# Kernel optimization log

Hardware: AMD Instinct MI355X
Metric: run time of the kernel (lower is better)

Reference implementation:

```python
import jax, jax.numpy as jnp
import numpy as np

N, E, B, H, W = 2048, 65536, 4, 64, 64
D, ED, HID, ATT, STEPS = 128, 128, 256, 16, 4
NODE_IN, EDGE_IN = 256, 64


def setup_inputs() -> dict:
    key = jax.random.key(0)
    ks = jax.random.split(key, 24)
    p = lambda k, s: jax.random.normal(k, s, jnp.float32) * 0.05
    z = lambda n: jnp.zeros((n,), jnp.float32)
    return dict(
        x=jax.random.normal(ks[0], (N, NODE_IN), jnp.float32),
        edge_attr=jax.random.normal(ks[1], (E, EDGE_IN), jnp.float32),
        edge_index=jax.random.randint(ks[2], (2, E), 0, N),
        feature_maps=jax.random.normal(ks[3], (B, 32, H, W), jnp.float32),
        batch_index=jax.random.randint(ks[4], (N,), 0, B),
        ne_w=p(ks[5], (D, NODE_IN)), ne_b=z(D),
        ee_w=p(ks[6], (ED, EDGE_IN)), ee_b=z(ED),
        me_w1=p(ks[7], (HID, 2 * (D + ATT) + ED)), me_b1=z(HID),
        me_w2=p(ks[8], (ED, HID)), me_b2=z(ED),
        mn_w=p(ks[9], (D, D + ATT + ED)), mn_b=z(D),
        key_w=p(ks[10], (ATT, D)), key_b=z(ATT),
        q_w=p(ks[11], (ATT, 32)), q_b=z(ATT),
        v_w=p(ks[12], (ATT, 32)), v_b=z(ATT),
        ec_w1=p(ks[13], (64, ED)), ec_b1=z(64),
        ec_w2=p(ks[14], (1, 64)), ec_b2=z(1),
        nc_w1=p(ks[15], (64, D)), nc_b1=z(64),
        nc_w2=p(ks[16], (1, 64)), nc_b2=z(1),
        cl_w1=p(ks[17], (64, D)), cl_b1=z(64),
        cl_w2=p(ks[18], (17, 64)), cl_b2=z(17),
    )


def _forward(x, edge_attr, feature_maps, edge_index, batch_index,
             ne_w, ne_b, ee_w, ee_b, me_w1, me_b1, me_w2, me_b2, mn_w, mn_b,
             key_w, key_b, q_w, q_b, v_w, v_b,
             ec_w1, ec_b1, ec_w2, ec_b2, nc_w1, nc_b1, nc_w2, nc_b2,
             cl_w1, cl_b1, cl_w2, cl_b2):
    relu = jax.nn.relu
    node_features = relu(x @ ne_w.T + ne_b)            # [N, D]
    edge_features = relu(edge_attr @ ee_w.T + ee_b)    # [E, ED]
    fm = feature_maps.reshape(B, 32, H * W)
    queries = jnp.einsum('oc,bcp->bop', q_w, fm) + q_b[None, :, None]  # [B,ATT,HW]
    values = jnp.einsum('oc,bcp->bop', v_w, fm) + v_b[None, :, None]   # [B,ATT,HW]
    src, tgt = edge_index[0], edge_index[1]  # j, i (messages aggregated at i)
    node_ids = jnp.arange(N)
    for _ in range(STEPS):
        k = node_features @ key_w.T + key_b                        # [N, ATT]
        attn = jax.nn.softmax(jnp.einsum('nk,bkp->bnp', k, queries), axis=2)
        result = jnp.einsum('bkp,bnp->bkn', values, attn)          # [B, ATT, N]
        res = result[batch_index, :, node_ids]                     # [N, ATT]
        nf = jnp.concatenate([node_features, res], axis=1)         # [N, D+ATT]
        x_i, x_j = nf[tgt], nf[src]
        edge_features = relu(relu(jnp.concatenate([x_i, x_j, edge_features], 1) @ me_w1.T + me_b1) @ me_w2.T + me_b2)
        msg = relu(jnp.concatenate([x_i, edge_features], 1) @ mn_w.T + mn_b)
        node_features = jax.ops.segment_sum(msg, tgt, num_segments=N)
    pe = (relu(edge_features @ ec_w1.T + ec_b1) @ ec_w2.T + ec_b2).squeeze(-1)
    pn = (relu(node_features @ nc_w1.T + nc_b1) @ nc_w2.T + nc_b2).squeeze(-1)
    pc = relu(node_features @ cl_w1.T + cl_b1) @ cl_w2.T + cl_b2
    return pe, pn, pc, node_features, edge_features


def reference(x, edge_attr, edge_index, feature_maps, batch_index,
              ne_w, ne_b, ee_w, ee_b, me_w1, me_b1, me_w2, me_b2, mn_w, mn_b,
              key_w, key_b, q_w, q_b, v_w, v_b,
              ec_w1, ec_b1, ec_w2, ec_b2, nc_w1, nc_b1, nc_w2, nc_b2,
              cl_w1, cl_b1, cl_w2, cl_b2):
    return _forward(x, edge_attr, feature_maps, edge_index, batch_index,
                    ne_w, ne_b, ee_w, ee_b, me_w1, me_b1, me_w2, me_b2, mn_w, mn_b,
                    key_w, key_b, q_w, q_b, v_w, v_b,
                    ec_w1, ec_b1, ec_w2, ec_b2, nc_w1, nc_b1, nc_w2, nc_b2,
                    cl_w1, cl_b1, cl_w2, cl_b2)
```

## Files before the change

kernel.cpp:

```cpp
#include <hip/hip_runtime.h>

#define N_NODES 2048
#define N_EDGES 65536
#define BATCH   4
#define PPIX    4096
#define STEPS   4

typedef __attribute__((ext_vector_type(4))) float f32x4;
typedef __attribute__((ext_vector_type(8))) short s16x8;

__device__ __forceinline__ unsigned short f2bf(float f) {
    unsigned u = __float_as_uint(f);
    unsigned r = u + 0x7fffu + ((u >> 16) & 1u);
    return (unsigned short)(r >> 16);
}
__device__ __forceinline__ float bf2f(unsigned short h) {
    return __uint_as_float(((unsigned)h) << 16);
}

__global__ __launch_bounds__(256) void k_hist(const int* __restrict__ ei,
                                              const int* __restrict__ batch_ix,
                                              int* __restrict__ hist,
                                              int* __restrict__ bcnt) {
    int i = blockIdx.x * 256 + threadIdx.x;
    if (i < N_EDGES) atomicAdd(&hist[ei[N_EDGES + i]], 1);
    if (i < N_NODES) atomicAdd(&bcnt[batch_ix[i]], 1);
}

__global__ __launch_bounds__(256) void k_scan(const int* __restrict__ hist,
                                              const int* __restrict__ bcnt,
                                              int* __restrict__ cursor,
                                              int* __restrict__ boff,
                                              int* __restrict__ bcur) {
    __shared__ int tls[256];
    const int t = threadIdx.x;
    int loc[8];
    int s = 0;
#pragma unroll
    for (int j = 0; j < 8; j++) { loc[j] = s; s += hist[t * 8 + j]; }
    tls[t] = s;
    __syncthreads();
    for (int off = 1; off < 256; off <<= 1) {
        int v = (t >= off) ? tls[t - off] : 0;
        __syncthreads();
        tls[t] += v;
        __syncthreads();
    }
    int base = (t > 0) ? tls[t - 1] : 0;
#pragma unroll
    for (int j = 0; j < 8; j++) cursor[t * 8 + j] = base + loc[j];
    if (t == 0) {
        int b = 0;
        for (int i = 0; i < 4; i++) { boff[i] = b; bcur[i] = b; b += bcnt[i]; }
    }
}

__global__ __launch_bounds__(256) void k_scatter(const int* __restrict__ ei,
                                                 const int* __restrict__ batch_ix,
                                                 int* __restrict__ cursor, int* __restrict__ bcur,
                                                 int* __restrict__ perm, int* __restrict__ nperm) {
    int i = blockIdx.x * 256 + threadIdx.x;
    if (i < N_EDGES) {
        int pos = atomicAdd(&cursor[ei[N_EDGES + i]], 1);
        perm[pos] = i;
    }
    if (i < N_NODES) {
        int pos = atomicAdd(&bcur[batch_ix[i]], 1);
        nperm[pos] = i;
    }
}

__global__ void k_wconv(const float* __restrict__ w1, const float* __restrict__ w2,
                        const float* __restrict__ w3, const float* __restrict__ ec1,
                        unsigned short* __restrict__ o1, unsigned short* __restrict__ o2,
                        unsigned short* __restrict__ o3, unsigned short* __restrict__ o4) {
    int i = blockIdx.x * 256 + threadIdx.x;
    if (i < 256 * 416) o1[i] = f2bf(w1[i]);
    if (i < 128 * 256) o2[i] = f2bf(w2[i]);
    if (i < 128 * 288) {
        int r = i / 288, c = i - r * 288;
        o3[i] = (c < 272) ? f2bf(w3[r * 272 + c]) : (unsigned short)0;
    }
    if (i < 64 * 128) o4[i] = f2bf(ec1[i]);
}

__global__ __launch_bounds__(128) void k_node_enc(const float* __restrict__ x,
                                                  const float* __restrict__ w,
                                                  const float* __restrict__ b,
                                                  float* __restrict__ out) {
    __shared__ float xs[256];
    const int n = blockIdx.x;
    for (int i = threadIdx.x; i < 256; i += 128) xs[i] = x[n * 256 + i];
    __syncthreads();
    const int d = threadIdx.x;
    const float* wr = w + d * 256;
    float acc = b[d];
#pragma unroll 8
    for (int c = 0; c < 256; c++) acc += xs[c] * wr[c];
    out[n * 128 + d] = fmaxf(acc, 0.f);
}

__global__ __launch_bounds__(256) void k_edge_enc(const float* __restrict__ ea,
                                                  const float* __restrict__ w,
                                                  const float* __restrict__ b,
                                                  const int* __restrict__ perm,
                                                  unsigned short* __restrict__ ef) {
    __shared__ float ws[128 * 64];
    __shared__ float bs[128];
    for (int i = threadIdx.x; i < 128 * 64; i += 256) ws[i] = w[i];
    if (threadIdx.x < 128) bs[threadIdx.x] = b[threadIdx.x];
    __syncthreads();
    const int slot = blockIdx.x * 256 + threadIdx.x;
    const int e = perm[slot];
    float xr[64];
#pragma unroll
    for (int c = 0; c < 64; c++) xr[c] = ea[(size_t)e * 64 + c];
    for (int d = 0; d < 128; d++) {
        float acc = bs[d];
        const float* wr = &ws[d * 64];
#pragma unroll
        for (int c = 0; c < 64; c++) acc += xr[c] * wr[c];
        ef[(size_t)slot * 128 + d] = f2bf(fmaxf(acc, 0.f));
    }
}

__global__ __launch_bounds__(256) void k_qv(const float* __restrict__ fm,
                                            const float* __restrict__ qw, const float* __restrict__ qb,
                                            const float* __restrict__ vw, const float* __restrict__ vb,
                                            float* __restrict__ q, float* __restrict__ v) {
    __shared__ float fs[32][256];
    const int b = blockIdx.x >> 4;
    const int pt = blockIdx.x & 15;
    for (int i = threadIdx.x; i < 32 * 256; i += 256) {
        int c = i >> 8, p = i & 255;
        fs[c][p] = fm[(size_t)b * 32 * PPIX + (size_t)c * PPIX + pt * 256 + p];
    }
    __syncthreads();
    const int p = threadIdx.x;
    for (int o = 0; o < 16; o++) {
        float qa = qb[o], va = vb[o];
#pragma unroll
        for (int c = 0; c < 32; c++) {
            float f = fs[c][p];
            qa += qw[o * 32 + c] * f;
            va += vw[o * 32 + c] * f;
        }
        size_t oidx = ((size_t)b * 16 + o) * PPIX + pt * 256 + p;
        q[oidx] = qa;
        v[oidx] = va;
    }
}

__global__ __launch_bounds__(256) void k_attn(const float* __restrict__ nf,
                                              const float* __restrict__ qbuf,
                                              const float* __restrict__ vbuf,
                                              const float* __restrict__ key_w,
                                              const float* __restrict__ key_b,
                                              const int* __restrict__ nperm,
                                              const int* __restrict__ boff,
                                              const int* __restrict__ bcnt,
                                              unsigned short* __restrict__ nf_bf,
                                              float* __restrict__ nxt) {
    const int b = blockIdx.x >> 9;
    const int chunk = blockIdx.x & 511;
    const int cnt = bcnt[b];
    if (chunk * 4 >= cnt) return;
    const int base = boff[b] + chunk * 4;
    const int nvalid = min(4, cnt - chunk * 4);
    const int t = threadIdx.x;

    __shared__ int nid[4];
    __shared__ float xs[4][128];
    __shared__ float ks[4][16];
    __shared__ float pbuf[4][4][18];

    if (t < 4) nid[t] = nperm[base + ((t < nvalid) ? t : 0)];
    __syncthreads();
    for (int i2 = t; i2 < 4 * 128; i2 += 256) {
        int i = i2 >> 7, d = i2 & 127;
        xs[i][d] = nf[(size_t)nid[i] * 128 + d];
        if (i < nvalid) nxt[(size_t)nid[i] * 128 + d] = 0.f;
    }
    __syncthreads();
    if (t < 64) {
        int i = t >> 4, a = t & 15;
        const float* wr = key_w + a * 128;
        float acc = key_b[a];
#pragma unroll 8
        for (int c = 0; c < 128; c++) acc += xs[i][c] * wr[c];
        ks[i][a] = acc;
    }
    __syncthreads();

    const float* q = qbuf + (size_t)b * 16 * PPIX;
    const float* v = vbuf + (size_t)b * 16 * PPIX;

    float m[4], wsm[4], vacc[4][16];
#pragma unroll
    for (int i = 0; i < 4; i++) {
        m[i] = -1e30f; wsm[i] = 0.f;
#pragma unroll
        for (int a = 0; a < 16; a++) vacc[i][a] = 0.f;
    }

    for (int ch = 0; ch < 16; ch++) {
        int p = ch * 256 + t;
        float qv[16], vv[16];
#pragma unroll
        for (int a = 0; a < 16; a++) qv[a] = q[a * PPIX + p];
#pragma unroll
        for (int a = 0; a < 16; a++) vv[a] = v[a * PPIX + p];
#pragma unroll
        for (int i = 0; i < 4; i++) {
            float s = 0.f;
#pragma unroll
            for (int a = 0; a < 16; a++) s += ks[i][a] * qv[a];
            if (s > m[i]) {
                float sc = __expf(m[i] - s);
                wsm[i] *= sc;
#pragma unroll
                for (int a = 0; a < 16; a++) vacc[i][a] *= sc;
                m[i] = s;
            }
            float w = __expf(s - m[i]);
            wsm[i] += w;
#pragma unroll
            for (int a = 0; a < 16; a++) vacc[i][a] += w * vv[a];
        }
    }

    for (int off = 1; off < 64; off <<= 1) {
#pragma unroll
        for (int i = 0; i < 4; i++) {
            float mo = __shfl_xor(m[i], off);
            float wo = __shfl_xor(wsm[i], off);
            float mn = fmaxf(m[i], mo);
            float se = __expf(m[i] - mn), so = __expf(mo - mn);
            wsm[i] = wsm[i] * se + wo * so;
#pragma unroll
            for (int a = 0; a < 16; a++) {
                float vo = __shfl_xor(vacc[i][a], off);
                vacc[i][a] = vacc[i][a] * se + vo * so;
            }
            m[i] = mn;
        }
    }
    const int wv = t >> 6;
    if ((t & 63) == 0) {
#pragma unroll
        for (int i = 0; i < 4; i++) {
            pbuf[wv][i][0] = m[i];
            pbuf[wv][i][1] = wsm[i];
#pragma unroll
            for (int a = 0; a < 16; a++) pbuf[wv][i][2 + a] = vacc[i][a];
        }
    }
    __syncthreads();
    if (t < 64) {
        int i = t >> 4, a = t & 15;
        float mg = fmaxf(fmaxf(pbuf[0][i][0], pbuf[1][i][0]), fmaxf(pbuf[2][i][0], pbuf[3][i][0]));
        float num = 0.f, den = 0.f;
#pragma unroll
        for (int w = 0; w < 4; w++) {
            float f = __expf(pbuf[w][i][0] - mg);
            num += pbuf[w][i][2 + a] * f;
            den += pbuf[w][i][1] * f;
        }
        if (i < nvalid) nf_bf[(size_t)nid[i] * 144 + 128 + a] = f2bf(num / den);
    }
    for (int i2 = t; i2 < 4 * 128; i2 += 256) {
        int i = i2 >> 7, d = i2 & 127;
        if (i < nvalid) nf_bf[(size_t)nid[i] * 144 + d] = f2bf(xs[i][d]);
    }
}

__global__ __launch_bounds__(512, 4) void k_mlp(const unsigned short* __restrict__ nf_bf,
                                                unsigned short* __restrict__ ef_buf,
                                                const unsigned short* __restrict__ w1b,
                                                const unsigned short* __restrict__ w2b,
                                                const unsigned short* __restrict__ w3b,
                                                const float* __restrict__ me_b1,
                                                const float* __restrict__ me_b2,
                                                const float* __restrict__ mn_b,
                                                const int* __restrict__ ei,
                                                const int* __restrict__ perm,
                                                float* __restrict__ node_acc) {
    __shared__ __attribute__((aligned(16))) unsigned short catA[64 * 424];
    __shared__ int tgt_s[64];
    __shared__ int src_s[64];
    const int tid = threadIdx.x;
    const int e0 = blockIdx.x * 64;
    const int* srcI = ei;
    const int* tgtI = ei + N_EDGES;
    if (tid < 64) {
        int eg = perm[e0 + tid];
        tgt_s[tid] = tgtI[eg];
        src_s[tid] = srcI[eg];
    }
    __syncthreads();
    for (int c = tid; c < 64 * 52; c += 512) {
        int e = c / 52;
        int r = c - e * 52;
        const unsigned short* sp;
        int dcol;
        if (r < 18)      { sp = nf_bf + (size_t)tgt_s[e] * 144 + r * 8;        dcol = r * 8; }
        else if (r < 36) { sp = nf_bf + (size_t)src_s[e] * 144 + (r - 18) * 8; dcol = 144 + (r - 18) * 8; }
        else             { sp = ef_buf + (size_t)(e0 + e) * 128 + (r - 36) * 8; dcol = 288 + (r - 36) * 8; }
        *(s16x8*)&catA[e * 424 + dcol] = *(const s16x8*)sp;
    }
    __syncthreads();

    const int lane = tid & 63;
    const int wid = tid >> 6;
    const int wm = wid >> 2;
    const int wn = wid & 3;
    const int lr = lane & 15;
    const int lk = lane >> 4;
    const int rbase = wm * 32;
    const f32x4 z4 = {0.f, 0.f, 0.f, 0.f};

    f32x4 acc[2][4];
    for (int mt = 0; mt < 2; mt++)
        for (int nt = 0; nt < 4; nt++) acc[mt][nt] = z4;
#pragma unroll 2
    for (int kc = 0; kc < 13; kc++) {
        s16x8 a0 = *(const s16x8*)&catA[(rbase + lr) * 424 + kc * 32 + lk * 8];
        s16x8 a1 = *(const s16x8*)&catA[(rbase + 16 + lr) * 424 + kc * 32 + lk * 8];
#pragma unroll
        for (int nt = 0; nt < 4; nt++) {
            int nn = wn * 64 + nt * 16 + lr;
            s16x8 b = *(const s16x8*)&w1b[(size_t)nn * 416 + kc * 32 + lk * 8];
            acc[0][nt] = __builtin_amdgcn_mfma_f32_16x16x32_bf16(a0, b, acc[0][nt], 0, 0, 0);
            acc[1][nt] = __builtin_amdgcn_mfma_f32_16x16x32_bf16(a1, b, acc[1][nt], 0, 0, 0);
        }
    }
    __syncthreads();
#pragma unroll
    for (int nt = 0; nt < 4; nt++) {
        int nn = wn * 64 + nt * 16 + lr;
        float bias = me_b1[nn];
#pragma unroll
        for (int mt = 0; mt < 2; mt++)
#pragma unroll
            for (int r = 0; r < 4; r++) {
                int m = rbase + mt * 16 + lk * 4 + r;
                catA[m * 424 + 144 + nn] = f2bf(fmaxf(acc[mt][nt][r] + bias, 0.f));
            }
    }
    __syncthreads();

    f32x4 acc2[2][2];
    for (int mt = 0; mt < 2; mt++)
        for (int nt = 0; nt < 2; nt++) acc2[mt][nt] = z4;
#pragma unroll 2
    for (int kc = 0; kc < 8; kc++) {
        s16x8 a0 = *(const s16x8*)&catA[(rbase + lr) * 424 + 144 + kc * 32 + lk * 8];
        s16x8 a1 = *(const s16x8*)&catA[(rbase + 16 + lr) * 424 + 144 + kc * 32 + lk * 8];
#pragma unroll
        for (int nt = 0; nt < 2; nt++) {
            int nn = wn * 32 + nt * 16 + lr;
            s16x8 b = *(const s16x8*)&w2b[(size_t)nn * 256 + kc * 32 + lk * 8];
            acc2[0][nt] = __builtin_amdgcn_mfma_f32_16x16x32_bf16(a0, b, acc2[0][nt], 0, 0, 0);
            acc2[1][nt] = __builtin_amdgcn_mfma_f32_16x16x32_bf16(a1, b, acc2[1][nt], 0, 0, 0);
        }
    }
    __syncthreads();
#pragma unroll
    for (int nt = 0; nt < 2; nt++) {
        int nn = wn * 32 + nt * 16 + lr;
        float bias = me_b2[nn];
#pragma unroll
        for (int mt = 0; mt < 2; mt++)
#pragma unroll
            for (int r = 0; r < 4; r++) {
                int m = rbase + mt * 16 + lk * 4 + r;
                catA[m * 424 + 144 + nn] = f2bf(fmaxf(acc2[mt][nt][r] + bias, 0.f));
            }
    }
    __syncthreads();

    f32x4 acc3[2][2];
    for (int mt = 0; mt < 2; mt++)
        for (int nt = 0; nt < 2; nt++) acc3[mt][nt] = z4;
#pragma unroll 2
    for (int kc = 0; kc < 9; kc++) {
        s16x8 a0 = *(const s16x8*)&catA[(rbase + lr) * 424 + kc * 32 + lk * 8];
        s16x8 a1 = *(const s16x8*)&catA[(rbase + 16 + lr) * 424 + kc * 32 + lk * 8];
#pragma unroll
        for (int nt = 0; nt < 2; nt++) {
            int nn = wn * 32 + nt * 16 + lr;
            s16x8 b = *(const s16x8*)&w3b[(size_t)nn * 288 + kc * 32 + lk * 8];
            acc3[0][nt] = __builtin_amdgcn_mfma_f32_16x16x32_bf16(a0, b, acc3[0][nt], 0, 0, 0);
            acc3[1][nt] = __builtin_amdgcn_mfma_f32_16x16x32_bf16(a1, b, acc3[1][nt], 0, 0, 0);
        }
    }
    __syncthreads();
#pragma unroll
    for (int nt = 0; nt < 2; nt++) {
        int nn = wn * 32 + nt * 16 + lr;
        float bias = mn_b[nn];
#pragma unroll
        for (int mt = 0; mt < 2; mt++)
#pragma unroll
            for (int r = 0; r < 4; r++) {
                int m = rbase + mt * 16 + lk * 4 + r;
                *(float*)&catA[m * 424 + 144 + nn * 2] = fmaxf(acc3[mt][nt][r] + bias, 0.f);
            }
    }
    __syncthreads();
    {
        const int c = tid & 127;
        const int r0 = (tid >> 7) * 16;
        float run = *(const float*)&catA[r0 * 424 + 144 + c * 2];
        int prev = tgt_s[r0];
        for (int r = r0 + 1; r < r0 + 16; r++) {
            int tg = tgt_s[r];
            float val = *(const float*)&catA[r * 424 + 144 + c * 2];
            if (tg != prev) {
                atomicAdd(&node_acc[(size_t)prev * 128 + c], run);
                run = val;
                prev = tg;
            } else {
                run += val;
            }
        }
        atomicAdd(&node_acc[(size_t)prev * 128 + c], run);
    }
#pragma unroll
    for (int nt = 0; nt < 2; nt++) {
        int nn = wn * 32 + nt * 16 + lr;
        float bias = me_b2[nn];
#pragma unroll
        for (int mt = 0; mt < 2; mt++)
#pragma unroll
            for (int r = 0; r < 4; r++) {
                int m = rbase + mt * 16 + lk * 4 + r;
                ef_buf[(size_t)(e0 + m) * 128 + nn] = f2bf(fmaxf(acc2[mt][nt][r] + bias, 0.f));
            }
    }
}

__global__ __launch_bounds__(256) void k_edge_head(const unsigned short* __restrict__ ef,
                                                   const unsigned short* __restrict__ w1b,
                                                   const float* __restrict__ b1,
                                                   const float* __restrict__ w2,
                                                   const float* __restrict__ b2,
                                                   const int* __restrict__ perm,
                                                   float* __restrict__ pe,
                                                   float* __restrict__ ef_out) {
    __shared__ __attribute__((aligned(16))) unsigned short efs[32][136];
    __shared__ float h_s[32][68];
    __shared__ int ep_s[32];
    const int tid = threadIdx.x;
    const int e0 = blockIdx.x * 32;
    if (tid < 32) ep_s[tid] = perm[e0 + tid];
    __syncthreads();
    for (int c = tid; c < 32 * 16; c += 256) {
        int e = c >> 4, r = c & 15;
        s16x8 v = *(const s16x8*)&ef[(size_t)(e0 + e) * 128 + r * 8];
        *(s16x8*)&efs[e][r * 8] = v;
        float4 lo, hi;
        lo.x = bf2f((unsigned short)v[0]); lo.y = bf2f((unsigned short)v[1]);
        lo.z = bf2f((unsigned short)v[2]); lo.w = bf2f((unsigned short)v[3]);
        hi.x = bf2f((unsigned short)v[4]); hi.y = bf2f((unsigned short)v[5]);
        hi.z = bf2f((unsigned short)v[6]); hi.w = bf2f((unsigned short)v[7]);
        size_t ob = (size_t)ep_s[e] * 128 + r * 8;
        *(float4*)&ef_out[ob] = lo;
        *(float4*)&ef_out[ob + 4] = hi;
    }
    __syncthreads();
    const int lane = tid & 63;
    const int wid = tid >> 6;
    const int lr = lane & 15;
    const int lk = lane >> 4;
    const f32x4 z4 = {0.f, 0.f, 0.f, 0.f};
    f32x4 acc0 = z4, acc1 = z4;
    for (int kc = 0; kc < 4; kc++) {
        s16x8 a0 = *(const s16x8*)&efs[lr][kc * 32 + lk * 8];
        s16x8 a1 = *(const s16x8*)&efs[16 + lr][kc * 32 + lk * 8];
        s16x8 b = *(const s16x8*)&w1b[(size_t)(wid * 16 + lr) * 128 + kc * 32 + lk * 8];
        acc0 = __builtin_amdgcn_mfma_f32_16x16x32_bf16(a0, b, acc0, 0, 0, 0);
        acc1 = __builtin_amdgcn_mfma_f32_16x16x32_bf16(a1, b, acc1, 0, 0, 0);
    }
    {
        int h = wid * 16 + lr;
        float bias = b1[h];
#pragma unroll
        for (int r = 0; r < 4; r++) {
            h_s[lk * 4 + r][h]      = fmaxf(acc0[r] + bias, 0.f);
            h_s[16 + lk * 4 + r][h] = fmaxf(acc1[r] + bias, 0.f);
        }
    }
    __syncthreads();
    if (tid < 32) {
        float a = b2[0];
#pragma unroll 8
        for (int h = 0; h < 64; h++) a += w2[h] * h_s[tid][h];
        pe[ep_s[tid]] = a;
    }
}

__global__ __launch_bounds__(64) void k_node_heads(const float* __restrict__ nf,
                                                   const float* __restrict__ nc_w1, const float* __restrict__ nc_b1,
                                                   const float* __restrict__ nc_w2, const float* __restrict__ nc_b2,
                                                   const float* __restrict__ cl_w1, const float* __restrict__ cl_b1,
                                                   const float* __restrict__ cl_w2, const float* __restrict__ cl_b2,
                                                   float* __restrict__ pn, float* __restrict__ pc,
                                                   float* __restrict__ nf_out) {
    __shared__ float xs[128];
    __shared__ float hr2[64];
    const int n = blockIdx.x;
    const int t = threadIdx.x;
    float2 xv = *(const float2*)&nf[(size_t)n * 128 + t * 2];
    xs[t * 2] = xv.x;
    xs[t * 2 + 1] = xv.y;
    *(float2*)&nf_out[(size_t)n * 128 + t * 2] = xv;
    __syncthreads();
    float a1 = nc_b1[t], a2 = cl_b1[t];
#pragma unroll 8
    for (int d4 = 0; d4 < 32; d4++) {
        float4 w1v = *(const float4*)&nc_w1[(size_t)t * 128 + d4 * 4];
        float4 w2v = *(const float4*)&cl_w1[(size_t)t * 128 + d4 * 4];
        float x0 = xs[d4 * 4], x1 = xs[d4 * 4 + 1], x2 = xs[d4 * 4 + 2], x3 = xs[d4 * 4 + 3];
        a1 += x0 * w1v.x + x1 * w1v.y + x2 * w1v.z + x3 * w1v.w;
        a2 += x0 * w2v.x + x1 * w2v.y + x2 * w2v.z + x3 * w2v.w;
    }
    float h1 = fmaxf(a1, 0.f);
    hr2[t] = fmaxf(a2, 0.f);
    float p = nc_w2[t] * h1;
#pragma unroll
    for (int off = 32; off > 0; off >>= 1) p += __shfl_down(p, off);
    if (t == 0) pn[n] = p + nc_b2[0];
    __syncthreads();
    if (t < 17) {
        float a = cl_b2[t];
#pragma unroll 8
        for (int h = 0; h < 64; h++) a += cl_w2[t * 64 + h] * hr2[h];
        pc[(size_t)n * 17 + t] = a;
    }
}

extern "C" void kernel_launch(void* const* d_in, const int* in_sizes, int n_in,
                              void* d_out, int out_size, void* d_ws, size_t ws_size,
                              hipStream_t stream) {
    const float* x         = (const float*)d_in[0];
    const float* edge_attr = (const float*)d_in[1];
    const int*   edge_idx  = (const int*)d_in[2];
    const float* fmaps     = (const float*)d_in[3];
    const int*   batch_ix  = (const int*)d_in[4];
    const float* ne_w  = (const float*)d_in[5];
    const float* ne_b  = (const float*)d_in[6];
    const float* ee_w  = (const float*)d_in[7];
    const float* ee_b  = (const float*)d_in[8];
    const float* me_w1 = (const float*)d_in[9];
    const float* me_b1 = (const float*)d_in[10];
    const float* me_w2 = (const float*)d_in[11];
    const float* me_b2 = (const float*)d_in[12];
    const float* mn_w  = (const float*)d_in[13];
    const float* mn_b  = (const float*)d_in[14];
    const float* key_w = (const float*)d_in[15];
    const float* key_b = (const float*)d_in[16];
    const float* q_w   = (const float*)d_in[17];
    const float* q_b   = (const float*)d_in[18];
    const float* v_w   = (const float*)d_in[19];
    const float* v_b   = (const float*)d_in[20];
    const float* ec_w1 = (const float*)d_in[21];
    const float* ec_b1 = (const float*)d_in[22];
    const float* ec_w2 = (const float*)d_in[23];
    const float* ec_b2 = (const float*)d_in[24];
    const float* nc_w1 = (const float*)d_in[25];
    const float* nc_b1 = (const float*)d_in[26];
    const float* nc_w2 = (const float*)d_in[27];
    const float* nc_b2 = (const float*)d_in[28];
    const float* cl_w1 = (const float*)d_in[29];
    const float* cl_b1 = (const float*)d_in[30];
    const float* cl_w2 = (const float*)d_in[31];
    const float* cl_b2 = (const float*)d_in[32];

    char* wsp = (char*)d_ws;
    size_t off = 0;
    auto alloc = [&](size_t bytes) -> void* {
        void* p = wsp + off;
        off += (bytes + 255) & ~(size_t)255;
        return p;
    };
    float* q_buf = (float*)alloc((size_t)BATCH * 16 * PPIX * sizeof(float));
    float* v_buf = (float*)alloc((size_t)BATCH * 16 * PPIX * sizeof(float));
    float* nfA   = (float*)alloc((size_t)N_NODES * 128 * sizeof(float));
    float* nfB   = (float*)alloc((size_t)N_NODES * 128 * sizeof(float));
    unsigned short* nf_bf  = (unsigned short*)alloc((size_t)N_NODES * 144 * 2);
    unsigned short* ef_buf = (unsigned short*)alloc((size_t)N_EDGES * 128 * 2);
    unsigned short* w1b = (unsigned short*)alloc(256 * 416 * 2);
    unsigned short* w2b = (unsigned short*)alloc(128 * 256 * 2);
    unsigned short* w3b = (unsigned short*)alloc(128 * 288 * 2);
    unsigned short* w4b = (unsigned short*)alloc(64 * 128 * 2);
    int* hist   = (int*)alloc((2048 + 4) * sizeof(int));
    int* bcnt   = hist + 2048;
    int* cursor = (int*)alloc(2048 * sizeof(int));
    int* boff   = (int*)alloc(4 * sizeof(int));
    int* bcur   = (int*)alloc(4 * sizeof(int));
    int* perm   = (int*)alloc((size_t)N_EDGES * sizeof(int));
    int* nperm  = (int*)alloc((size_t)N_NODES * sizeof(int));

    float* pe_out = (float*)d_out;
    float* pn_out = pe_out + N_EDGES;
    float* pc_out = pn_out + N_NODES;
    float* nf_out = pc_out + (size_t)N_NODES * 17;
    float* ef_out = nf_out + (size_t)N_NODES * 128;

    hipMemsetAsync(hist, 0, (2048 + 4) * sizeof(int), stream);
    k_hist<<<N_EDGES / 256, 256, 0, stream>>>(edge_idx, batch_ix, hist, bcnt);
    k_scan<<<1, 256, 0, stream>>>(hist, bcnt, cursor, boff, bcur);
    k_scatter<<<N_EDGES / 256, 256, 0, stream>>>(edge_idx, batch_ix, cursor, bcur, perm, nperm);

    k_wconv<<<416, 256, 0, stream>>>(me_w1, me_w2, mn_w, ec_w1, w1b, w2b, w3b, w4b);
    k_node_enc<<<N_NODES, 128, 0, stream>>>(x, ne_w, ne_b, nfA);
    k_qv<<<64, 256, 0, stream>>>(fmaps, q_w, q_b, v_w, v_b, q_buf, v_buf);
    k_edge_enc<<<N_EDGES / 256, 256, 0, stream>>>(edge_attr, ee_w, ee_b, perm, ef_buf);

    float* cur = nfA;
    float* nxt = nfB;
    for (int step = 0; step < STEPS; step++) {
        k_attn<<<BATCH * 512, 256, 0, stream>>>(cur, q_buf, v_buf, key_w, key_b,
                                                nperm, boff, bcnt, nf_bf, nxt);
        k_mlp<<<N_EDGES / 64, 512, 0, stream>>>(nf_bf, ef_buf, w1b, w2b, w3b,
                                                me_b1, me_b2, mn_b, edge_idx, perm, nxt);
        float* tmp = cur; cur = nxt; nxt = tmp;
    }

    k_edge_head<<<N_EDGES / 32, 256, 0, stream>>>(ef_buf, w4b, ec_b1, ec_w2, ec_b2, perm, pe_out, ef_out);
    k_node_heads<<<N_NODES, 64, 0, stream>>>(cur, nc_w1, nc_b1, nc_w2, nc_b2,
                                             cl_w1, cl_b1, cl_w2, cl_b2, pn_out, pc_out, nf_out);
}
```

Baseline: 790.4 us.

## Move node/edge encoders to bf16 MFMA and split attention softmax into two passes

Node and edge encoders now convert inputs and weights to bf16 and compute 64-row tiles with MFMA 16x16x32 instead of scalar per-thread FP32 dot products, which removes the large scalar FMA and per-thread register cost in the edge encoder. The attention kernel drops the online softmax with its per-pixel rescaling branch. It first computes all scores and a block max, then accumulates exp-weighted values in a second pass with plain sum reductions. This trades encoder precision (bf16 inputs) and extra registers for the stored scores in exchange for less exp and rescale work.

```diff
diff --git a/kernel.cpp b/kernel.cpp
--- a/kernel.cpp
+++ b/kernel.cpp
@@ -72,8 +72,10 @@
 
 __global__ void k_wconv(const float* __restrict__ w1, const float* __restrict__ w2,
                         const float* __restrict__ w3, const float* __restrict__ ec1,
+                        const float* __restrict__ eew, const float* __restrict__ new_,
                         unsigned short* __restrict__ o1, unsigned short* __restrict__ o2,
-                        unsigned short* __restrict__ o3, unsigned short* __restrict__ o4) {
+                        unsigned short* __restrict__ o3, unsigned short* __restrict__ o4,
+                        unsigned short* __restrict__ o5, unsigned short* __restrict__ o6) {
     int i = blockIdx.x * 256 + threadIdx.x;
     if (i < 256 * 416) o1[i] = f2bf(w1[i]);
     if (i < 128 * 256) o2[i] = f2bf(w2[i]);
@@ -82,45 +84,142 @@
         o3[i] = (c < 272) ? f2bf(w3[r * 272 + c]) : (unsigned short)0;
     }
     if (i < 64 * 128) o4[i] = f2bf(ec1[i]);
-}
-
-__global__ __launch_bounds__(128) void k_node_enc(const float* __restrict__ x,
-                                                  const float* __restrict__ w,
+    if (i < 128 * 64) o5[i] = f2bf(eew[i]);
+    if (i < 128 * 256) o6[i] = f2bf(new_[i]);
+}
+
+__global__ __launch_bounds__(256) void k_node_enc(const float* __restrict__ x,
+                                                  const unsigned short* __restrict__ wb,
                                                   const float* __restrict__ b,
                                                   float* __restrict__ out) {
-    __shared__ float xs[256];
-    const int n = blockIdx.x;
-    for (int i = threadIdx.x; i < 256; i += 128) xs[i] = x[n * 256 + i];
-    __syncthreads();
-    const int d = threadIdx.x;
-    const float* wr = w + d * 256;
-    float acc = b[d];
-#pragma unroll 8
-    for (int c = 0; c < 256; c++) acc += xs[c] * wr[c];
-    out[n * 128 + d] = fmaxf(acc, 0.f);
+    __shared__ __attribute__((aligned(16))) unsigned short xs2[64 * 264];
+    const int tid = threadIdx.x;
+    const int n0 = blockIdx.x * 64;
+    {
+        int row = tid >> 2, qq = tid & 3;
+        const float* rp = x + (size_t)(n0 + row) * 256 + qq * 64;
+        unsigned short* dp = &xs2[row * 264 + qq * 64];
+#pragma unroll
+        for (int j = 0; j < 4; j++) {
+            float4 f0 = *(const float4*)(rp + j * 16 + 0);
+            float4 f1 = *(const float4*)(rp + j * 16 + 4);
+            float4 f2 = *(const float4*)(rp + j * 16 + 8);
+            float4 f3 = *(const float4*)(rp + j * 16 + 12);
+            s16x8 lo, hi;
+            lo[0] = (short)f2bf(f0.x); lo[1] = (short)f2bf(f0.y); lo[2] = (short)f2bf(f0.z); lo[3] = (short)f2bf(f0.w);
+            lo[4] = (short)f2bf(f1.x); lo[5] = (short)f2bf(f1.y); lo[6] = (short)f2bf(f1.z); lo[7] = (short)f2bf(f1.w);
+            hi[0] = (short)f2bf(f2.x); hi[1] = (short)f2bf(f2.y); hi[2] = (short)f2bf(f2.z); hi[3] = (short)f2bf(f2.w);
+            hi[4] = (short)f2bf(f3.x); hi[5] = (short)f2bf(f3.y); hi[6] = (short)f2bf(f3.z); hi[7] = (short)f2bf(f3.w);
+            *(s16x8*)(dp + j * 16) = lo;
+            *(s16x8*)(dp + j * 16 + 8) = hi;
+        }
+    }
+    __syncthreads();
+    const int lane = tid & 63;
+    const int wn = tid >> 6;
+    const int lr = lane & 15;
+    const int lk = lane >> 4;
+    const f32x4 z4 = {0.f, 0.f, 0.f, 0.f};
+    f32x4 acc[4][2];
+#pragma unroll
+    for (int mt = 0; mt < 4; mt++)
+#pragma unroll
+        for (int nt = 0; nt < 2; nt++) acc[mt][nt] = z4;
+#pragma unroll
+    for (int kc = 0; kc < 8; kc++) {
+        s16x8 a0 = *(const s16x8*)&xs2[(0 + lr) * 264 + kc * 32 + lk * 8];
+        s16x8 a1 = *(const s16x8*)&xs2[(16 + lr) * 264 + kc * 32 + lk * 8];
+        s16x8 a2 = *(const s16x8*)&xs2[(32 + lr) * 264 + kc * 32 + lk * 8];
+        s16x8 a3 = *(const s16x8*)&xs2[(48 + lr) * 264 + kc * 32 + lk * 8];
+#pragma unroll
+        for (int nt = 0; nt < 2; nt++) {
+            int nn = wn * 32 + nt * 16 + lr;
+            s16x8 bf = *(const s16x8*)&wb[(size_t)nn * 256 + kc * 32 + lk * 8];
+            acc[0][nt] = __builtin_amdgcn_mfma_f32_16x16x32_bf16(a0, bf, acc[0][nt], 0, 0, 0);
+            acc[1][nt] = __builtin_amdgcn_mfma_f32_16x16x32_bf16(a1, bf, acc[1][nt], 0, 0, 0);
+            acc[2][nt] = __builtin_amdgcn_mfma_f32_16x16x32_bf16(a2, bf, acc[2][nt], 0, 0, 0);
+            acc[3][nt] = __builtin_amdgcn_mfma_f32_16x16x32_bf16(a3, bf, acc[3][nt], 0, 0, 0);
+        }
+    }
+#pragma unroll
+    for (int nt = 0; nt < 2; nt++) {
+        int nn = wn * 32 + nt * 16 + lr;
+        float bias = b[nn];
+#pragma unroll
+        for (int mt = 0; mt < 4; mt++)
+#pragma unroll
+            for (int r = 0; r < 4; r++) {
+                int m = mt * 16 + lk * 4 + r;
+                out[(size_t)(n0 + m) * 128 + nn] = fmaxf(acc[mt][nt][r] + bias, 0.f);
+            }
+    }
 }
 
 __global__ __launch_bounds__(256) void k_edge_enc(const float* __restrict__ ea,
-                                                  const float* __restrict__ w,
+                                                  const unsigned short* __restrict__ wb,
                                                   const float* __restrict__ b,
                                                   const int* __restrict__ perm,
                                                   unsigned short* __restrict__ ef) {
-    __shared__ float ws[128 * 64];
-    __shared__ float bs[128];
-    for (int i = threadIdx.x; i < 128 * 64; i += 256) ws[i] = w[i];
-    if (threadIdx.x < 128) bs[threadIdx.x] = b[threadIdx.x];
-    __syncthreads();
-    const int slot = blockIdx.x * 256 + threadIdx.x;
-    const int e = perm[slot];
-    float xr[64];
-#pragma unroll
-    for (int c = 0; c < 64; c++) xr[c] = ea[(size_t)e * 64 + c];
-    for (int d = 0; d < 128; d++) {
-        float acc = bs[d];
-        const float* wr = &ws[d * 64];
-#pragma unroll
-        for (int c = 0; c < 64; c++) acc += xr[c] * wr[c];
-        ef[(size_t)slot * 128 + d] = f2bf(fmaxf(acc, 0.f));
+    __shared__ __attribute__((aligned(16))) unsigned short eas[64 * 72];
+    __shared__ int ep[64];
+    const int tid = threadIdx.x;
+    const int e0 = blockIdx.x * 64;
+    if (tid < 64) ep[tid] = perm[e0 + tid];
+    __syncthreads();
+    {
+        int row = tid >> 2, qq = tid & 3;
+        const float* rp = ea + (size_t)ep[row] * 64 + qq * 16;
+        float4 f0 = *(const float4*)(rp + 0);
+        float4 f1 = *(const float4*)(rp + 4);
+        float4 f2 = *(const float4*)(rp + 8);
+        float4 f3 = *(const float4*)(rp + 12);
+        s16x8 lo, hi;
+        lo[0] = (short)f2bf(f0.x); lo[1] = (short)f2bf(f0.y); lo[2] = (short)f2bf(f0.z); lo[3] = (short)f2bf(f0.w);
+        lo[4] = (short)f2bf(f1.x); lo[5] = (short)f2bf(f1.y); lo[6] = (short)f2bf(f1.z); lo[7] = (short)f2bf(f1.w);
+        hi[0] = (short)f2bf(f2.x); hi[1] = (short)f2bf(f2.y); hi[2] = (short)f2bf(f2.z); hi[3] = (short)f2bf(f2.w);
+        hi[4] = (short)f2bf(f3.x); hi[5] = (short)f2bf(f3.y); hi[6] = (short)f2bf(f3.z); hi[7] = (short)f2bf(f3.w);
+        unsigned short* dp = &eas[row * 72 + qq * 16];
+        *(s16x8*)(dp) = lo;
+        *(s16x8*)(dp + 8) = hi;
+    }
+    __syncthreads();
+    const int lane = tid & 63;
+    const int wn = tid >> 6;
+    const int lr = lane & 15;
+    const int lk = lane >> 4;
+    const f32x4 z4 = {0.f, 0.f, 0.f, 0.f};
+    f32x4 acc[4][2];
+#pragma unroll
+    for (int mt = 0; mt < 4; mt++)
+#pragma unroll
+        for (int nt = 0; nt < 2; nt++) acc[mt][nt] = z4;
+#pragma unroll
+    for (int kc = 0; kc < 2; kc++) {
+        s16x8 a0 = *(const s16x8*)&eas[(0 + lr) * 72 + kc * 32 + lk * 8];
+        s16x8 a1 = *(const s16x8*)&eas[(16 + lr) * 72 + kc * 32 + lk * 8];
+        s16x8 a2 = *(const s16x8*)&eas[(32 + lr) * 72 + kc * 32 + lk * 8];
+        s16x8 a3 = *(const s16x8*)&eas[(48 + lr) * 72 + kc * 32 + lk * 8];
+#pragma unroll
+        for (int nt = 0; nt < 2; nt++) {
+            int nn = wn * 32 + nt * 16 + lr;
+            s16x8 bf = *(const s16x8*)&wb[(size_t)nn * 64 + kc * 32 + lk * 8];
+            acc[0][nt] = __builtin_amdgcn_mfma_f32_16x16x32_bf16(a0, bf, acc[0][nt], 0, 0, 0);
+            acc[1][nt] = __builtin_amdgcn_mfma_f32_16x16x32_bf16(a1, bf, acc[1][nt], 0, 0, 0);
+            acc[2][nt] = __builtin_amdgcn_mfma_f32_16x16x32_bf16(a2, bf, acc[2][nt], 0, 0, 0);
+            acc[3][nt] = __builtin_amdgcn_mfma_f32_16x16x32_bf16(a3, bf, acc[3][nt], 0, 0, 0);
+        }
+    }
+#pragma unroll
+    for (int nt = 0; nt < 2; nt++) {
+        int nn = wn * 32 + nt * 16 + lr;
+        float bias = b[nn];
+#pragma unroll
+        for (int mt = 0; mt < 4; mt++)
+#pragma unroll
+            for (int r = 0; r < 4; r++) {
+                int m = mt * 16 + lk * 4 + r;
+                ef[(size_t)(e0 + m) * 128 + nn] = f2bf(fmaxf(acc[mt][nt][r] + bias, 0.f));
+            }
     }
 }
 
@@ -172,7 +271,8 @@
     __shared__ int nid[4];
     __shared__ float xs[4][128];
     __shared__ float ks[4][16];
-    __shared__ float pbuf[4][4][18];
+    __shared__ float redm[4][4];
+    __shared__ float pbuf[4][4][17];
 
     if (t < 4) nid[t] = nperm[base + ((t < nvalid) ? t : 0)];
     __syncthreads();
@@ -191,81 +291,88 @@
         ks[i][a] = acc;
     }
     __syncthreads();
+    float kk[4][16];
+#pragma unroll
+    for (int i = 0; i < 4; i++)
+#pragma unroll
+        for (int a = 0; a < 16; a++) kk[i][a] = ks[i][a];
 
     const float* q = qbuf + (size_t)b * 16 * PPIX;
     const float* v = vbuf + (size_t)b * 16 * PPIX;
 
-    float m[4], wsm[4], vacc[4][16];
-#pragma unroll
-    for (int i = 0; i < 4; i++) {
-        m[i] = -1e30f; wsm[i] = 0.f;
-#pragma unroll
-        for (int a = 0; a < 16; a++) vacc[i][a] = 0.f;
-    }
-
+    float s[4][16];
+    float m[4] = {-3e38f, -3e38f, -3e38f, -3e38f};
+#pragma unroll
     for (int ch = 0; ch < 16; ch++) {
         int p = ch * 256 + t;
-        float qv[16], vv[16];
+        float qv[16];
 #pragma unroll
         for (int a = 0; a < 16; a++) qv[a] = q[a * PPIX + p];
 #pragma unroll
-        for (int a = 0; a < 16; a++) vv[a] = v[a * PPIX + p];
-#pragma unroll
         for (int i = 0; i < 4; i++) {
-            float s = 0.f;
-#pragma unroll
-            for (int a = 0; a < 16; a++) s += ks[i][a] * qv[a];
-            if (s > m[i]) {
-                float sc = __expf(m[i] - s);
-                wsm[i] *= sc;
-#pragma unroll
-                for (int a = 0; a < 16; a++) vacc[i][a] *= sc;
-                m[i] = s;
-            }
-            float w = __expf(s - m[i]);
-            wsm[i] += w;
-#pragma unroll
-            for (int a = 0; a < 16; a++) vacc[i][a] += w * vv[a];
-        }
-    }
-
-    for (int off = 1; off < 64; off <<= 1) {
-#pragma unroll
-        for (int i = 0; i < 4; i++) {
-            float mo = __shfl_xor(m[i], off);
-            float wo = __shfl_xor(wsm[i], off);
-            float mn = fmaxf(m[i], mo);
-            float se = __expf(m[i] - mn), so = __expf(mo - mn);
-            wsm[i] = wsm[i] * se + wo * so;
-#pragma unroll
-            for (int a = 0; a < 16; a++) {
-                float vo = __shfl_xor(vacc[i][a], off);
-                vacc[i][a] = vacc[i][a] * se + vo * so;
-            }
-            m[i] = mn;
-        }
-    }
+            float acc = 0.f;
+#pragma unroll
+            for (int a = 0; a < 16; a++) acc += kk[i][a] * qv[a];
+            s[i][ch] = acc;
+            m[i] = fmaxf(m[i], acc);
+        }
+    }
+#pragma unroll
+    for (int off = 1; off < 64; off <<= 1)
+#pragma unroll
+        for (int i = 0; i < 4; i++) m[i] = fmaxf(m[i], __shfl_xor(m[i], off));
     const int wv = t >> 6;
     if ((t & 63) == 0) {
 #pragma unroll
+        for (int i = 0; i < 4; i++) redm[wv][i] = m[i];
+    }
+    __syncthreads();
+    float mf[4];
+#pragma unroll
+    for (int i = 0; i < 4; i++)
+        mf[i] = fmaxf(fmaxf(redm[0][i], redm[1][i]), fmaxf(redm[2][i], redm[3][i]));
+
+    float wsm[4] = {0.f, 0.f, 0.f, 0.f};
+    float vacc[4][16];
+#pragma unroll
+    for (int i = 0; i < 4; i++)
+#pragma unroll
+        for (int a = 0; a < 16; a++) vacc[i][a] = 0.f;
+#pragma unroll
+    for (int ch = 0; ch < 16; ch++) {
+        int p = ch * 256 + t;
+        float vv[16];
+#pragma unroll
+        for (int a = 0; a < 16; a++) vv[a] = v[a * PPIX + p];
+#pragma unroll
         for (int i = 0; i < 4; i++) {
-            pbuf[wv][i][0] = m[i];
-            pbuf[wv][i][1] = wsm[i];
-#pragma unroll
-            for (int a = 0; a < 16; a++) pbuf[wv][i][2 + a] = vacc[i][a];
+            float w = __expf(s[i][ch] - mf[i]);
+            wsm[i] += w;
+#pragma unroll
+            for (int a = 0; a < 16; a++) vacc[i][a] += w * vv[a];
+        }
+    }
+#pragma unroll
+    for (int off = 1; off < 64; off <<= 1)
+#pragma unroll
+        for (int i = 0; i < 4; i++) {
+            wsm[i] += __shfl_xor(wsm[i], off);
+#pragma unroll
+            for (int a = 0; a < 16; a++) vacc[i][a] += __shfl_xor(vacc[i][a], off);
+        }
+    if ((t & 63) == 0) {
+#pragma unroll
+        for (int i = 0; i < 4; i++) {
+            pbuf[wv][i][0] = wsm[i];
+#pragma unroll
+            for (int a = 0; a < 16; a++) pbuf[wv][i][1 + a] = vacc[i][a];
         }
     }
     __syncthreads();
     if (t < 64) {
         int i = t >> 4, a = t & 15;
-        float mg = fmaxf(fmaxf(pbuf[0][i][0], pbuf[1][i][0]), fmaxf(pbuf[2][i][0], pbuf[3][i][0]));
-        float num = 0.f, den = 0.f;
-#pragma unroll
-        for (int w = 0; w < 4; w++) {
-            float f = __expf(pbuf[w][i][0] - mg);
-            num += pbuf[w][i][2 + a] * f;
-            den += pbuf[w][i][1] * f;
-        }
+        float den = pbuf[0][i][0] + pbuf[1][i][0] + pbuf[2][i][0] + pbuf[3][i][0];
+        float num = pbuf[0][i][1 + a] + pbuf[1][i][1 + a] + pbuf[2][i][1 + a] + pbuf[3][i][1 + a];
         if (i < nvalid) nf_bf[(size_t)nid[i] * 144 + 128 + a] = f2bf(num / den);
     }
     for (int i2 = t; i2 < 4 * 128; i2 += 256) {
@@ -594,6 +701,8 @@
     unsigned short* w2b = (unsigned short*)alloc(128 * 256 * 2);
     unsigned short* w3b = (unsigned short*)alloc(128 * 288 * 2);
     unsigned short* w4b = (unsigned short*)alloc(64 * 128 * 2);
+    unsigned short* w5b = (unsigned short*)alloc(128 * 64 * 2);
+    unsigned short* w6b = (unsigned short*)alloc(128 * 256 * 2);
     int* hist   = (int*)alloc((2048 + 4) * sizeof(int));
     int* bcnt   = hist + 2048;
     int* cursor = (int*)alloc(2048 * sizeof(int));
@@ -613,10 +722,11 @@
     k_scan<<<1, 256, 0, stream>>>(hist, bcnt, cursor, boff, bcur);
     k_scatter<<<N_EDGES / 256, 256, 0, stream>>>(edge_idx, batch_ix, cursor, bcur, perm, nperm);
 
-    k_wconv<<<416, 256, 0, stream>>>(me_w1, me_w2, mn_w, ec_w1, w1b, w2b, w3b, w4b);
-    k_node_enc<<<N_NODES, 128, 0, stream>>>(x, ne_w, ne_b, nfA);
+    k_wconv<<<416, 256, 0, stream>>>(me_w1, me_w2, mn_w, ec_w1, ee_w, ne_w,
+                                     w1b, w2b, w3b, w4b, w5b, w6b);
+    k_node_enc<<<N_NODES / 64, 256, 0, stream>>>(x, w6b, ne_b, nfA);
     k_qv<<<64, 256, 0, stream>>>(fmaps, q_w, q_b, v_w, v_b, q_buf, v_buf);
-    k_edge_enc<<<N_EDGES / 256, 256, 0, stream>>>(edge_attr, ee_w, ee_b, perm, ef_buf);
+    k_edge_enc<<<N_EDGES / 64, 256, 0, stream>>>(edge_attr, w5b, ee_b, perm, ef_buf);
 
     float* cur = nfA;
     float* nxt = nfB;
```

Measured after the change: 732.6 us. 1.08x faster.
